# Kernel tuning notes

Measured on AMD Instinct MI355X. Metric: run time of the kernel, lower is better.

The kernel has to match this reference:

```python
import jax, jax.numpy as jnp
import numpy as np

B, T, C, H = 4, 2048, 768, 12
D = C // H  # head_size = 64
ROPE_BASE = 10000.0


def rotary_tables(seq_len, dim, dtype=jnp.float32):
    # dim = head_size; uses dim//2 frequencies
    inv_freq = 1.0 / (ROPE_BASE ** (jnp.arange(0, dim, 2, dtype=jnp.float32) / dim))
    t = jnp.arange(seq_len, dtype=jnp.float32)
    freqs = jnp.outer(t, inv_freq)  # [T, D/2]
    return jnp.cos(freqs).astype(dtype), jnp.sin(freqs).astype(dtype)


def apply_rotary(x, cos, sin):
    # x: [B, H, T, D]; cos/sin: [T, D/2] broadcast over B,H
    d = x.shape[-1] // 2
    x1, x2 = x[..., :d], x[..., d:]
    y1 = x1 * cos + x2 * sin
    y2 = -x1 * sin + x2 * cos
    return jnp.concatenate([y1, y2], axis=-1)


def setup_inputs() -> dict:
    key = jax.random.key(0)
    ks = jax.random.split(key, 5)
    x = jax.random.normal(ks[0], (B, T, C), dtype=jnp.float32)
    W_attn = jax.random.normal(ks[1], (C, 3 * C), dtype=jnp.float32) * (1.0 / np.sqrt(C))
    b_attn = jax.random.normal(ks[2], (3 * C,), dtype=jnp.float32) * 0.02
    W_proj = jax.random.normal(ks[3], (C, C), dtype=jnp.float32) * (1.0 / np.sqrt(C))
    b_proj = jax.random.normal(ks[4], (C,), dtype=jnp.float32) * 0.02
    return {"x": x, "W_attn": W_attn, "b_attn": b_attn, "W_proj": W_proj, "b_proj": b_proj}


def reference(x, W_attn, b_attn, W_proj, b_proj):
    Bx, Tx, Cx = x.shape
    qkv = x @ W_attn + b_attn  # [B, T, 3C]
    q, k, v = jnp.split(qkv, 3, axis=-1)
    # [B, T, C] -> [B, H, T, D]
    to_heads = lambda a: a.reshape(Bx, Tx, H, D).transpose(0, 2, 1, 3)
    q, k, v = to_heads(q), to_heads(k), to_heads(v)
    cos, sin = rotary_tables(Tx, D, x.dtype)
    q = apply_rotary(q, cos, sin)
    k = apply_rotary(k, cos, sin)
    scale = 1.0 / np.sqrt(D)
    scores = jnp.einsum('bhqd,bhkd->bhqk', q, k) * scale  # [B, H, T, T]
    causal = jnp.tril(jnp.ones((Tx, Tx), dtype=bool))
    scores = jnp.where(causal, scores, jnp.finfo(scores.dtype).min)
    attn = jax.nn.softmax(scores, axis=-1)
    y = jnp.einsum('bhqk,bhkd->bhqd', attn, v)  # [B, H, T, D]
    y = y.transpose(0, 2, 1, 3).reshape(Bx, Tx, Cx)
    return y @ W_proj + b_proj
```

## Files before the change

### kernel.cpp

```cpp
#include <hip/hip_runtime.h>
#include <hip/hip_bf16.h>

#define BB 4
#define TT 2048
#define CC 768
#define HH 12
#define DD 64
#define MM (BB * TT)
#define BH (BB * HH)

typedef __bf16 bf16_t;
typedef __bf16 bf16x8 __attribute__((ext_vector_type(8)));
typedef __bf16 bf16x4 __attribute__((ext_vector_type(4)));
typedef float f32x4 __attribute__((ext_vector_type(4)));

__device__ __forceinline__ float fast_exp2(float x) {
#if __has_builtin(__builtin_amdgcn_exp2f)
    return __builtin_amdgcn_exp2f(x);
#else
    return exp2f(x);
#endif
}

__device__ __forceinline__ uint32_t pk2(float lo, float hi) {
    bf16_t l = (bf16_t)lo, h = (bf16_t)hi;
    uint16_t lu = __builtin_bit_cast(uint16_t, l);
    uint16_t hu = __builtin_bit_cast(uint16_t, h);
    return ((uint32_t)hu << 16) | lu;
}

__device__ __forceinline__ void gload_lds16(const void* g, void* l) {
    __builtin_amdgcn_global_load_lds(
        (const __attribute__((address_space(1))) uint32_t*)g,
        (__attribute__((address_space(3))) uint32_t*)l, 16, 0, 0);
}

__global__ void cvt_f32_bf16(const float* __restrict__ in, bf16_t* __restrict__ out, int n4) {
    int tid = blockIdx.x * blockDim.x + threadIdx.x;
    if (tid >= n4) return;
    float4 v = ((const float4*)in)[tid];
    bf16x4 o;
    o[0] = (bf16_t)v.x; o[1] = (bf16_t)v.y; o[2] = (bf16_t)v.z; o[3] = (bf16_t)v.w;
    ((bf16x4*)out)[tid] = o;
}

__global__ void transpose_cvt(const float* __restrict__ W, bf16_t* __restrict__ WT, int K, int N) {
    __shared__ bf16_t tile[32][33];
    int k0 = blockIdx.x * 32, n0 = blockIdx.y * 32;
    int tx = threadIdx.x, ty = threadIdx.y;
#pragma unroll
    for (int r = 0; r < 4; ++r) {
        int kl = ty * 4 + r;
        tile[kl][tx] = (bf16_t)W[(size_t)(k0 + kl) * N + n0 + tx];
    }
    __syncthreads();
#pragma unroll
    for (int r = 0; r < 4; ++r) {
        int nl = ty * 4 + r;
        WT[(size_t)(n0 + nl) * K + k0 + tx] = tile[tx][nl];
    }
}

#define GEMM_CORE(A_, BT_, acc_)                                                       \
    __shared__ bf16_t As[2][128 * 32];                                                 \
    __shared__ bf16_t Bs[2][128 * 32];                                                 \
    int tid = threadIdx.x;                                                             \
    int wv = tid >> 6, lane = tid & 63, c = lane & 15, quad = lane >> 4;               \
    int wm = (wv >> 1) * 64, wn = (wv & 1) * 64;                                       \
    int m0 = blockIdx.x * 128, n0 = blockIdx.y * 128;                                  \
    int srow = wv * 32 + (lane >> 2);                                                  \
    int slot = lane & 3;                                                               \
    auto stage = [&](int buf, int k0) {                                                \
        _Pragma("unroll")                                                              \
        for (int ins = 0; ins < 2; ++ins) {                                            \
            int r = srow + ins * 16;                                                   \
            int g = (slot - ((r >> 1) & 3)) & 3;                                       \
            const bf16_t* ga = A_ + (size_t)(m0 + r) * K + k0 + g * 8;                 \
            const bf16_t* gb = BT_ + (size_t)(n0 + r) * K + k0 + g * 8;                \
            gload_lds16(ga, &As[buf][(wv * 32 + ins * 16) * 32]);                      \
            gload_lds16(gb, &Bs[buf][(wv * 32 + ins * 16) * 32]);                      \
        }                                                                              \
    };                                                                                 \
    int s_rd = (quad + ((c >> 1) & 3)) & 3;                                            \
    const int nk = K / 32;                                                             \
    stage(0, 0);                                                                       \
    for (int kt = 0; kt < nk; ++kt) {                                                  \
        __syncthreads();                                                               \
        if (kt + 1 < nk) stage((kt + 1) & 1, (kt + 1) * 32);                           \
        int buf = kt & 1;                                                              \
        bf16x8 af[4], bfr[4];                                                          \
        _Pragma("unroll")                                                              \
        for (int i = 0; i < 4; ++i) af[i] = *(const bf16x8*)&As[buf][(wm + i * 16 + c) * 32 + s_rd * 8];  \
        _Pragma("unroll")                                                              \
        for (int j = 0; j < 4; ++j) bfr[j] = *(const bf16x8*)&Bs[buf][(wn + j * 16 + c) * 32 + s_rd * 8]; \
        _Pragma("unroll")                                                              \
        for (int i = 0; i < 4; ++i)                                                    \
            _Pragma("unroll")                                                          \
            for (int j = 0; j < 4; ++j)                                                \
                acc_[i][j] = __builtin_amdgcn_mfma_f32_16x16x32_bf16(af[i], bfr[j], acc_[i][j], 0, 0, 0); \
    }

__global__ __launch_bounds__(256, 3) void gemm_qkv(
        const bf16_t* __restrict__ A, const bf16_t* __restrict__ BT,
        const float* __restrict__ bias,
        bf16_t* __restrict__ Qh, bf16_t* __restrict__ Kh, bf16_t* __restrict__ Vt) {
    const int K = 768;
    __shared__ __align__(16) bf16_t smem[17408];
    bf16_t* Asp = smem;
    bf16_t* Bsp = smem + 8192;
    int tid = threadIdx.x;
    int wv = tid >> 6, lane = tid & 63, c = lane & 15, quad = lane >> 4;
    int wm = (wv >> 1) * 64, wn = (wv & 1) * 64;
    int m0 = blockIdx.x * 128, n0 = blockIdx.y * 128;
    int srow = wv * 32 + (lane >> 2);
    int slot = lane & 3;
    auto stage = [&](int buf, int k0) {
#pragma unroll
        for (int ins = 0; ins < 2; ++ins) {
            int r = srow + ins * 16;
            int g = (slot - ((r >> 1) & 3)) & 3;
            gload_lds16(A + (size_t)(m0 + r) * K + k0 + g * 8, &Asp[buf * 4096 + (wv * 32 + ins * 16) * 32]);
            gload_lds16(BT + (size_t)(n0 + r) * K + k0 + g * 8, &Bsp[buf * 4096 + (wv * 32 + ins * 16) * 32]);
        }
    };
    int s_rd = (quad + ((c >> 1) & 3)) & 3;
    f32x4 acc[4][4] = {};
    const int nk = K / 32;
    stage(0, 0);
    for (int kt = 0; kt < nk; ++kt) {
        __syncthreads();
        if (kt + 1 < nk) stage((kt + 1) & 1, (kt + 1) * 32);
        int buf = kt & 1;
        bf16x8 af[4], bfr[4];
#pragma unroll
        for (int i = 0; i < 4; ++i) af[i] = *(const bf16x8*)&Asp[buf * 4096 + (wm + i * 16 + c) * 32 + s_rd * 8];
#pragma unroll
        for (int j = 0; j < 4; ++j) bfr[j] = *(const bf16x8*)&Bsp[buf * 4096 + (wn + j * 16 + c) * 32 + s_rd * 8];
#pragma unroll
        for (int i = 0; i < 4; ++i)
#pragma unroll
            for (int j = 0; j < 4; ++j)
                acc[i][j] = __builtin_amdgcn_mfma_f32_16x16x32_bf16(af[i], bfr[j], acc[i][j], 0, 0, 0);
    }
    __syncthreads();

    int type = n0 / 768;
    int hloc = ((n0 % 768) + wn) >> 6;
    int bidx = m0 >> 11;
    int colb = n0 + wn;
    int tb = (m0 + wm) & (TT - 1);
    bf16_t* epi = smem + wv * 4352;
    int rrow = lane >> 3, cchunk = lane & 7;

    if (type < 2) {
        const float rscale = (type == 0) ? 0.125f * 1.44269504088896f : 1.0f;
#pragma unroll
        for (int j = 0; j < 2; ++j) {
            int dlo = j * 16 + c;
            float infr = fast_exp2(-(float)dlo * 0.4152410118609828f);
            float blo = bias[colb + j * 16 + c];
            float bhi = bias[colb + (j + 2) * 16 + c];
#pragma unroll
            for (int i = 0; i < 4; ++i)
#pragma unroll
                for (int r = 0; r < 4; ++r) {
                    int lr = i * 16 + quad * 4 + r;
                    float a = acc[i][j][r] + blo;
                    float b2 = acc[i][j + 2][r] + bhi;
                    float fr = (float)(tb + lr) * infr;
                    float cs, sn;
                    __sincosf(fr, &sn, &cs);
                    epi[lr * 68 + dlo]      = (bf16_t)((a * cs + b2 * sn) * rscale);
                    epi[lr * 68 + dlo + 32] = (bf16_t)((-a * sn + b2 * cs) * rscale);
                }
        }
        bf16_t* dst = (type == 0 ? Qh : Kh) + (size_t)(bidx * HH + hloc) * TT * DD + (size_t)tb * DD;
#pragma unroll
        for (int it = 0; it < 8; ++it) {
            int row = it * 8 + rrow;
            bf16x8 v = *(const bf16x8*)&epi[row * 68 + cchunk * 8];
            *(bf16x8*)&dst[row * 64 + cchunk * 8] = v;
        }
    } else {
        int kt64 = tb >> 6;
#pragma unroll
        for (int j = 0; j < 4; ++j) {
            int dim = j * 16 + c;
            float bv = bias[colb + j * 16 + c];
            int rot = (dim & 7) * 8;
#pragma unroll
            for (int i = 0; i < 4; ++i)
#pragma unroll
                for (int r = 0; r < 4; ++r) {
                    int tin = i * 16 + quad * 4 + r;
                    epi[dim * 68 + ((tin + rot) & 63)] = (bf16_t)(acc[i][j][r] + bv);
                }
        }
        bf16_t* dstV = Vt + (size_t)(bidx * HH + hloc) * (TT / 64) * 4096 + (size_t)kt64 * 4096;
#pragma unroll
        for (int it = 0; it < 8; ++it) {
            int dim = it * 8 + rrow;
            int src = ((cchunk + (dim & 7)) & 7) * 8;
            bf16x8 v = *(const bf16x8*)&epi[dim * 68 + src];
            *(bf16x8*)&dstV[dim * 64 + cchunk * 8] = v;
        }
    }
}

__global__ __launch_bounds__(256, 3) void gemm_proj(
        const bf16_t* __restrict__ A, const bf16_t* __restrict__ BT,
        const float* __restrict__ bias, float* __restrict__ Cout) {
    const int K = 768;
    f32x4 acc[4][4] = {};
    GEMM_CORE(A, BT, acc)
#pragma unroll
    for (int j = 0; j < 4; ++j) {
        int col = n0 + wn + j * 16 + c;
        float bv = bias[col];
#pragma unroll
        for (int i = 0; i < 4; ++i) {
            int row = m0 + wm + i * 16 + quad * 4;
#pragma unroll
            for (int r = 0; r < 4; ++r)
                Cout[(size_t)(row + r) * CC + col] = acc[i][j][r] + bv;
        }
    }
}

__global__ __launch_bounds__(256, 3) void flash_attn(
        const bf16_t* __restrict__ Q, const bf16_t* __restrict__ Kc,
        const bf16_t* __restrict__ Vt, bf16_t* __restrict__ Y) {
    __shared__ bf16_t Ks[2][64 * 64];
    __shared__ bf16_t Vs[2][64 * 64];
    int blk = blockIdx.x;
    int r0 = (blk < 256) ? blk : ((blk < 512) ? (1023 - blk) : (blk - 256));
    int qt = 15 - (r0 / 48);
    int bh = r0 % 48;
    int wv = threadIdx.x >> 6, lane = threadIdx.x & 63;
    int b = bh / HH, h = bh - b * HH;
    int c = lane & 15, quad = lane >> 4;
    int qbw = qt * 128 + wv * 32;
    const bf16_t* Qg = Q + ((size_t)bh * TT + qbw) * DD;
    const bf16_t* Kg = Kc + (size_t)bh * TT * DD;
    const bf16_t* Vg = Vt + (size_t)bh * (TT / 64) * 4096;

    bf16x8 qf[2][2];
#pragma unroll
    for (int s = 0; s < 2; ++s)
#pragma unroll
        for (int ch = 0; ch < 2; ++ch)
            qf[s][ch] = *(const bf16x8*)(Qg + (s * 16 + c) * DD + ch * 32 + quad * 8);

    int srow = wv * 16 + (lane >> 3);
    int slot = lane & 7;
    auto stage = [&](int buf, int kt64) {
#pragma unroll
        for (int ins = 0; ins < 2; ++ins) {
            int r = srow + ins * 8;
            int g = (slot - (r & 7)) & 7;
            gload_lds16(Kg + (size_t)(kt64 * 64 + r) * 64 + g * 8, &Ks[buf][(wv * 16 + ins * 8) * 64]);
            gload_lds16(Vg + (size_t)kt64 * 4096 + r * 64 + g * 8, &Vs[buf][(wv * 16 + ins * 8) * 64]);
        }
    };

    f32x4 O[2][4] = {};
    float lsum[2] = {0.0f, 0.0f};
    int lane_lo = c + ((quad & 1) << 5);
    int lane_hi = lane_lo + 16;
    bool lowq = (quad < 2);

    int ntiles = 2 * qt + 2;
    stage(0, 0);
    for (int kt = 0; kt < ntiles; ++kt) {
        __syncthreads();
        if (kt + 1 < ntiles) stage((kt + 1) & 1, kt + 1);
        int buf = kt & 1;
#pragma unroll
        for (int t32 = 0; t32 < 2; ++t32) {
            int ks = kt * 64 + t32 * 32;
            if (ks > qbw) continue;
            bool masked = (ks == qbw);
            bf16x8 kf[2][2], vf[4];
#pragma unroll
            for (int t2 = 0; t2 < 2; ++t2)
#pragma unroll
                for (int ch = 0; ch < 2; ++ch) {
                    int row = t32 * 32 + t2 * 16 + c;
                    int sl = (ch * 4 + quad + (c & 7)) & 7;
                    kf[t2][ch] = *(const bf16x8*)&Ks[buf][row * 64 + sl * 8];
                }
#pragma unroll
            for (int nt = 0; nt < 4; ++nt) {
                int row = nt * 16 + c;
                int sl = (t32 * 4 + quad + (c & 7)) & 7;
                vf[nt] = *(const bf16x8*)&Vs[buf][row * 64 + sl * 8];
            }
            f32x4 st[2][2] = {};
#pragma unroll
            for (int s = 0; s < 2; ++s)
#pragma unroll
                for (int t2 = 0; t2 < 2; ++t2) {
                    st[s][t2] = __builtin_amdgcn_mfma_f32_16x16x32_bf16(kf[t2][0], qf[s][0], st[s][t2], 0, 0, 0);
                    st[s][t2] = __builtin_amdgcn_mfma_f32_16x16x32_bf16(kf[t2][1], qf[s][1], st[s][t2], 0, 0, 0);
                }
#pragma unroll
            for (int s = 0; s < 2; ++s) {
                float pv[2][4];
#pragma unroll
                for (int t2 = 0; t2 < 2; ++t2)
#pragma unroll
                    for (int r = 0; r < 4; ++r) {
                        float p = fast_exp2(st[s][t2][r]);
                        if (masked) {
                            int keyl = t2 * 16 + quad * 4 + r;
                            if (keyl > s * 16 + c) p = 0.0f;
                        }
                        pv[t2][r] = p;
                    }
                lsum[s] += ((pv[0][0] + pv[0][1]) + (pv[0][2] + pv[0][3]))
                         + ((pv[1][0] + pv[1][1]) + (pv[1][2] + pv[1][3]));
                uint32_t pk0a = pk2(pv[0][0], pv[0][1]), pk0b = pk2(pv[0][2], pv[0][3]);
                uint32_t pk1a = pk2(pv[1][0], pv[1][1]), pk1b = pk2(pv[1][2], pv[1][3]);
                union { uint32_t u[4]; bf16x8 v; } pf;
                {
                    uint32_t x0 = (uint32_t)__shfl((int)pk0a, lane_lo);
                    uint32_t y0 = (uint32_t)__shfl((int)pk1a, lane_lo);
                    pf.u[0] = lowq ? x0 : y0;
                    uint32_t x1 = (uint32_t)__shfl((int)pk0b, lane_lo);
                    uint32_t y1 = (uint32_t)__shfl((int)pk1b, lane_lo);
                    pf.u[1] = lowq ? x1 : y1;
                    uint32_t x2 = (uint32_t)__shfl((int)pk0a, lane_hi);
                    uint32_t y2 = (uint32_t)__shfl((int)pk1a, lane_hi);
                    pf.u[2] = lowq ? x2 : y2;
                    uint32_t x3 = (uint32_t)__shfl((int)pk0b, lane_hi);
                    uint32_t y3 = (uint32_t)__shfl((int)pk1b, lane_hi);
                    pf.u[3] = lowq ? x3 : y3;
                }
#pragma unroll
                for (int nt = 0; nt < 4; ++nt)
                    O[s][nt] = __builtin_amdgcn_mfma_f32_16x16x32_bf16(vf[nt], pf.v, O[s][nt], 0, 0, 0);
            }
        }
    }

#pragma unroll
    for (int s = 0; s < 2; ++s) {
        float l = lsum[s];
        l += __shfl_xor(l, 16);
        l += __shfl_xor(l, 32);
        float inv_l = 1.0f / l;
        int row = b * TT + qbw + s * 16 + c;
#pragma unroll
        for (int nt = 0; nt < 4; ++nt) {
            bf16x4 ov;
#pragma unroll
            for (int r = 0; r < 4; ++r) ov[r] = (bf16_t)(O[s][nt][r] * inv_l);
            *(bf16x4*)(Y + (size_t)row * CC + h * DD + nt * 16 + quad * 4) = ov;
        }
    }
}

extern "C" void kernel_launch(void* const* d_in, const int* in_sizes, int n_in,
                              void* d_out, int out_size, void* d_ws, size_t ws_size,
                              hipStream_t stream) {
    const float* x      = (const float*)d_in[0];
    const float* W_attn = (const float*)d_in[1];
    const float* b_attn = (const float*)d_in[2];
    const float* W_proj = (const float*)d_in[3];
    const float* b_proj = (const float*)d_in[4];
    float* out = (float*)d_out;

    unsigned char* ws = (unsigned char*)d_ws;
    size_t off = 0;
    auto alloc = [&](size_t bytes) { void* p = ws + off; off += (bytes + 255) & ~(size_t)255; return p; };
    bf16_t* xb  = (bf16_t*)alloc((size_t)MM * CC * 2);
    bf16_t* WaT = (bf16_t*)alloc((size_t)3 * CC * CC * 2);
    bf16_t* WpT = (bf16_t*)alloc((size_t)CC * CC * 2);
    bf16_t* Qh  = (bf16_t*)alloc((size_t)BH * TT * DD * 2);
    bf16_t* Kh  = (bf16_t*)alloc((size_t)BH * TT * DD * 2);
    bf16_t* Vt  = (bf16_t*)alloc((size_t)BH * TT * DD * 2);
    bf16_t* Yb  = (bf16_t*)alloc((size_t)MM * CC * 2);

    cvt_f32_bf16<<<(MM * CC / 4 + 255) / 256, 256, 0, stream>>>(x, xb, MM * CC / 4);
    transpose_cvt<<<dim3(CC / 32, 3 * CC / 32), dim3(32, 8), 0, stream>>>(W_attn, WaT, CC, 3 * CC);
    transpose_cvt<<<dim3(CC / 32, CC / 32), dim3(32, 8), 0, stream>>>(W_proj, WpT, CC, CC);
    gemm_qkv<<<dim3(MM / 128, 3 * CC / 128), 256, 0, stream>>>(xb, WaT, b_attn, Qh, Kh, Vt);
    flash_attn<<<dim3(768), 256, 0, stream>>>(Qh, Kh, Vt, Yb);
    gemm_proj<<<dim3(MM / 128, CC / 128), 256, 0, stream>>>(Yb, WpT, b_proj, out);
}
```

Baseline: 201.6 us.

## Switch flash attention to 32x32x16 MFMA tiles with permlane32 swap for P

Rewrites the attention inner loop to use 32x32x16 bf16 MFMA instructions instead of 16x16x32, with each wave computing one 32x32 score tile and two 32x32 output accumulators. The P-matrix relayout between the QK and PV MFMAs now uses v_permlane32_swap instead of eight cross-lane shuffles plus selects. The intent is fewer MFMA issues, fewer LDS fragment loads and cheaper register shuffling per tile. In exchange it relies on gfx950-specific permlane instructions and larger accumulator vectors, which raise register pressure.

```diff
diff --git a/kernel.cpp b/kernel.cpp
--- a/kernel.cpp
+++ b/kernel.cpp
@@ -13,6 +13,7 @@
 typedef __bf16 bf16x8 __attribute__((ext_vector_type(8)));
 typedef __bf16 bf16x4 __attribute__((ext_vector_type(4)));
 typedef float f32x4 __attribute__((ext_vector_type(4)));
+typedef float f32x16 __attribute__((ext_vector_type(16)));
 
 __device__ __forceinline__ float fast_exp2(float x) {
 #if __has_builtin(__builtin_amdgcn_exp2f)
@@ -238,18 +239,16 @@
     int bh = r0 % 48;
     int wv = threadIdx.x >> 6, lane = threadIdx.x & 63;
     int b = bh / HH, h = bh - b * HH;
-    int c = lane & 15, quad = lane >> 4;
+    int q31 = lane & 31, hi = lane >> 5;
     int qbw = qt * 128 + wv * 32;
     const bf16_t* Qg = Q + ((size_t)bh * TT + qbw) * DD;
     const bf16_t* Kg = Kc + (size_t)bh * TT * DD;
     const bf16_t* Vg = Vt + (size_t)bh * (TT / 64) * 4096;
 
-    bf16x8 qf[2][2];
-#pragma unroll
-    for (int s = 0; s < 2; ++s)
-#pragma unroll
-        for (int ch = 0; ch < 2; ++ch)
-            qf[s][ch] = *(const bf16x8*)(Qg + (s * 16 + c) * DD + ch * 32 + quad * 8);
+    bf16x8 qf[4];
+#pragma unroll
+    for (int dk = 0; dk < 4; ++dk)
+        qf[dk] = *(const bf16x8*)(Qg + (size_t)q31 * DD + dk * 16 + hi * 8);
 
     int srow = wv * 16 + (lane >> 3);
     int slot = lane & 7;
@@ -263,11 +262,8 @@
         }
     };
 
-    f32x4 O[2][4] = {};
-    float lsum[2] = {0.0f, 0.0f};
-    int lane_lo = c + ((quad & 1) << 5);
-    int lane_hi = lane_lo + 16;
-    bool lowq = (quad < 2);
+    f32x16 O[2] = {};
+    float lsum = 0.0f;
 
     int ntiles = 2 * qt + 2;
     stage(0, 0);
@@ -280,84 +276,73 @@
             int ks = kt * 64 + t32 * 32;
             if (ks > qbw) continue;
             bool masked = (ks == qbw);
-            bf16x8 kf[2][2], vf[4];
-#pragma unroll
-            for (int t2 = 0; t2 < 2; ++t2)
-#pragma unroll
-                for (int ch = 0; ch < 2; ++ch) {
-                    int row = t32 * 32 + t2 * 16 + c;
-                    int sl = (ch * 4 + quad + (c & 7)) & 7;
-                    kf[t2][ch] = *(const bf16x8*)&Ks[buf][row * 64 + sl * 8];
+
+            f32x16 st = {};
+#pragma unroll
+            for (int dk = 0; dk < 4; ++dk) {
+                int row = t32 * 32 + q31;
+                int sl = ((dk * 2 + hi) + (row & 7)) & 7;
+                bf16x8 kf = *(const bf16x8*)&Ks[buf][row * 64 + sl * 8];
+                st = __builtin_amdgcn_mfma_f32_32x32x16_bf16(kf, qf[dk], st, 0, 0, 0);
+            }
+
+            bf16x8 vf[2][2];
+#pragma unroll
+            for (int dt = 0; dt < 2; ++dt)
+#pragma unroll
+                for (int sli = 0; sli < 2; ++sli) {
+                    int row = dt * 32 + q31;
+                    int ch = t32 * 4 + sli * 2 + hi;
+                    int sl = (ch + (row & 7)) & 7;
+                    vf[dt][sli] = *(const bf16x8*)&Vs[buf][row * 64 + sl * 8];
                 }
-#pragma unroll
-            for (int nt = 0; nt < 4; ++nt) {
-                int row = nt * 16 + c;
-                int sl = (t32 * 4 + quad + (c & 7)) & 7;
-                vf[nt] = *(const bf16x8*)&Vs[buf][row * 64 + sl * 8];
+
+            float p[16];
+#pragma unroll
+            for (int r = 0; r < 16; ++r) {
+                float e = fast_exp2(st[r]);
+                if (masked) {
+                    int keyl = (r & 3) + 8 * (r >> 2) + 4 * hi;
+                    if (keyl > q31) e = 0.0f;
+                }
+                p[r] = e;
             }
-            f32x4 st[2][2] = {};
-#pragma unroll
-            for (int s = 0; s < 2; ++s)
-#pragma unroll
-                for (int t2 = 0; t2 < 2; ++t2) {
-                    st[s][t2] = __builtin_amdgcn_mfma_f32_16x16x32_bf16(kf[t2][0], qf[s][0], st[s][t2], 0, 0, 0);
-                    st[s][t2] = __builtin_amdgcn_mfma_f32_16x16x32_bf16(kf[t2][1], qf[s][1], st[s][t2], 0, 0, 0);
-                }
-#pragma unroll
-            for (int s = 0; s < 2; ++s) {
-                float pv[2][4];
-#pragma unroll
-                for (int t2 = 0; t2 < 2; ++t2)
-#pragma unroll
-                    for (int r = 0; r < 4; ++r) {
-                        float p = fast_exp2(st[s][t2][r]);
-                        if (masked) {
-                            int keyl = t2 * 16 + quad * 4 + r;
-                            if (keyl > s * 16 + c) p = 0.0f;
-                        }
-                        pv[t2][r] = p;
-                    }
-                lsum[s] += ((pv[0][0] + pv[0][1]) + (pv[0][2] + pv[0][3]))
-                         + ((pv[1][0] + pv[1][1]) + (pv[1][2] + pv[1][3]));
-                uint32_t pk0a = pk2(pv[0][0], pv[0][1]), pk0b = pk2(pv[0][2], pv[0][3]);
-                uint32_t pk1a = pk2(pv[1][0], pv[1][1]), pk1b = pk2(pv[1][2], pv[1][3]);
-                union { uint32_t u[4]; bf16x8 v; } pf;
-                {
-                    uint32_t x0 = (uint32_t)__shfl((int)pk0a, lane_lo);
-                    uint32_t y0 = (uint32_t)__shfl((int)pk1a, lane_lo);
-                    pf.u[0] = lowq ? x0 : y0;
-                    uint32_t x1 = (uint32_t)__shfl((int)pk0b, lane_lo);
-                    uint32_t y1 = (uint32_t)__shfl((int)pk1b, lane_lo);
-                    pf.u[1] = lowq ? x1 : y1;
-                    uint32_t x2 = (uint32_t)__shfl((int)pk0a, lane_hi);
-                    uint32_t y2 = (uint32_t)__shfl((int)pk1a, lane_hi);
-                    pf.u[2] = lowq ? x2 : y2;
-                    uint32_t x3 = (uint32_t)__shfl((int)pk0b, lane_hi);
-                    uint32_t y3 = (uint32_t)__shfl((int)pk1b, lane_hi);
-                    pf.u[3] = lowq ? x3 : y3;
-                }
-#pragma unroll
-                for (int nt = 0; nt < 4; ++nt)
-                    O[s][nt] = __builtin_amdgcn_mfma_f32_16x16x32_bf16(vf[nt], pf.v, O[s][nt], 0, 0, 0);
+            lsum += ((((p[0] + p[1]) + (p[2] + p[3])) + ((p[4] + p[5]) + (p[6] + p[7])))
+                  + (((p[8] + p[9]) + (p[10] + p[11])) + ((p[12] + p[13]) + (p[14] + p[15]))));
+
+            union { uint32_t u[4]; bf16x8 v; } pb[2];
+#pragma unroll
+            for (int sli = 0; sli < 2; ++sli) {
+                uint32_t a0 = pk2(p[sli * 8 + 0], p[sli * 8 + 1]);
+                uint32_t b0 = pk2(p[sli * 8 + 2], p[sli * 8 + 3]);
+                uint32_t a1 = pk2(p[sli * 8 + 4], p[sli * 8 + 5]);
+                uint32_t b1 = pk2(p[sli * 8 + 6], p[sli * 8 + 7]);
+                asm("v_permlane32_swap_b32 %0, %1" : "+v"(a0), "+v"(a1));
+                asm("v_permlane32_swap_b32 %0, %1" : "+v"(b0), "+v"(b1));
+                pb[sli].u[0] = a0; pb[sli].u[1] = b0; pb[sli].u[2] = a1; pb[sli].u[3] = b1;
             }
-        }
-    }
-
-#pragma unroll
-    for (int s = 0; s < 2; ++s) {
-        float l = lsum[s];
-        l += __shfl_xor(l, 16);
-        l += __shfl_xor(l, 32);
-        float inv_l = 1.0f / l;
-        int row = b * TT + qbw + s * 16 + c;
-#pragma unroll
-        for (int nt = 0; nt < 4; ++nt) {
+
+#pragma unroll
+            for (int dt = 0; dt < 2; ++dt) {
+                O[dt] = __builtin_amdgcn_mfma_f32_32x32x16_bf16(vf[dt][0], pb[0].v, O[dt], 0, 0, 0);
+                O[dt] = __builtin_amdgcn_mfma_f32_32x32x16_bf16(vf[dt][1], pb[1].v, O[dt], 0, 0, 0);
+            }
+        }
+    }
+
+    float l = lsum;
+    l += __shfl_xor(l, 32);
+    float inv_l = 1.0f / l;
+    int row = b * TT + qbw + q31;
+#pragma unroll
+    for (int dt = 0; dt < 2; ++dt)
+#pragma unroll
+        for (int g = 0; g < 4; ++g) {
             bf16x4 ov;
 #pragma unroll
-            for (int r = 0; r < 4; ++r) ov[r] = (bf16_t)(O[s][nt][r] * inv_l);
-            *(bf16x4*)(Y + (size_t)row * CC + h * DD + nt * 16 + quad * 4) = ov;
-        }
-    }
+            for (int r = 0; r < 4; ++r) ov[r] = (bf16_t)(O[dt][g * 4 + r] * inv_l);
+            *(bf16x4*)(Y + (size_t)row * CC + h * DD + dt * 32 + g * 8 + hi * 4) = ov;
+        }
 }
 
 extern "C" void kernel_launch(void* const* d_in, const int* in_sizes, int n_in,
```

Result: faster. 192.2 us (-4.7%).
